# Optimization experiments

Hardware: AMD Instinct MI355X
Metric: run time of the kernel (lower is better)

The kernel has to match this reference:

```python
import jax, jax.numpy as jnp
import numpy as np

DIM = 1024
DEPTH = 2
HEADS = 16
MLP = 4096
HEAD_DIM = DIM // HEADS
EPS = 1e-5


def layernorm(x, w, b):
    mu = jnp.mean(x, axis=-1, keepdims=True)
    var = jnp.mean(jnp.square(x - mu), axis=-1, keepdims=True)
    return (x - mu) * jax.lax.rsqrt(var + EPS) * w + b


def setup_inputs() -> dict:
    key = jax.random.key(0)
    ks = jax.random.split(key, 16)
    s = 0.02
    x = jax.random.normal(ks[0], (2, 2048, DIM), dtype=jnp.float32)
    inp = {
        "x": x,
        "ln1_w": jnp.ones((DEPTH, DIM), jnp.float32),
        "ln1_b": jnp.zeros((DEPTH, DIM), jnp.float32),
        "qkv_w": jax.random.normal(ks[1], (DEPTH, DIM, 3 * DIM), jnp.float32) * s,
        "qkv_b": jnp.zeros((DEPTH, 3 * DIM), jnp.float32),
        "in_w": jax.random.normal(ks[2], (DEPTH, DIM, 3 * DIM), jnp.float32) * s,
        "in_b": jnp.zeros((DEPTH, 3 * DIM), jnp.float32),
        "out_w": jax.random.normal(ks[3], (DEPTH, DIM, DIM), jnp.float32) * s,
        "out_b": jnp.zeros((DEPTH, DIM), jnp.float32),
        "ln2_w": jnp.ones((DEPTH, DIM), jnp.float32),
        "ln2_b": jnp.zeros((DEPTH, DIM), jnp.float32),
        "w1": jax.random.normal(ks[4], (DEPTH, DIM, MLP), jnp.float32) * s,
        "b1": jnp.zeros((DEPTH, MLP), jnp.float32),
        "w2": jax.random.normal(ks[5], (DEPTH, MLP, DIM), jnp.float32) * s,
        "b2": jnp.zeros((DEPTH, DIM), jnp.float32),
    }
    return inp


def _forward(x, ln1_w, ln1_b, qkv_w, qkv_b, in_w, in_b, out_w, out_b,
             ln2_w, ln2_b, w1, b1, w2, b2):
    B, S, D = x.shape
    scale = 1.0 / jnp.sqrt(jnp.float32(HEAD_DIM))
    for i in range(DEPTH):
        # --- Attention block (pre-norm) ---
        h = layernorm(x, ln1_w[i], ln1_b[i])
        qkv = h @ qkv_w[i] + qkv_b[i]                      # [B,S,3D]
        q, k, v = jnp.split(qkv, 3, axis=-1)
        # nn.MultiheadAttention's own in_proj on top of to_qkv
        qp = q @ in_w[i][:, :D] + in_b[i][:D]
        kp = k @ in_w[i][:, D:2 * D] + in_b[i][D:2 * D]
        vp = v @ in_w[i][:, 2 * D:] + in_b[i][2 * D:]
        qp = qp.reshape(B, S, HEADS, HEAD_DIM)
        kp = kp.reshape(B, S, HEADS, HEAD_DIM)
        vp = vp.reshape(B, S, HEADS, HEAD_DIM)
        scores = jnp.einsum("bqhd,bkhd->bhqk", qp, kp) * scale
        attn = jax.nn.softmax(scores, axis=-1)
        o = jnp.einsum("bhqk,bkhd->bqhd", attn, vp).reshape(B, S, D)
        o = o @ out_w[i] + out_b[i]
        x = o + x
        # --- FFN block (pre-norm) ---
        h = layernorm(x, ln2_w[i], ln2_b[i])
        h = jax.nn.gelu(h @ w1[i] + b1[i], approximate=False)
        h = h @ w2[i] + b2[i]
        x = h + x
    return x


def reference(x, ln1_w, ln1_b, qkv_w, qkv_b, in_w, in_b, out_w, out_b,
              ln2_w, ln2_b, w1, b1, w2, b2):
    return _forward(x, ln1_w, ln1_b, qkv_w, qkv_b, in_w, in_b, out_w, out_b,
                    ln2_w, ln2_b, w1, b1, w2, b2)
```

## Files before the change

kernel.cpp:

```cpp
#include <hip/hip_runtime.h>
#include <math.h>

#define D_MODEL 1024
#define NHEADS 16
#define HEAD_DIM 64
#define SEQ 2048
#define BATCH 2
#define TOK (BATCH*SEQ)
#define MLP_DIM 4096

#define F_BIAS  1
#define F_GELU  2
#define QSCALE 0.18033688011112042f

typedef __attribute__((ext_vector_type(8))) __bf16 bf16x8;
typedef __attribute__((ext_vector_type(16))) __bf16 bf16x16;
typedef __attribute__((ext_vector_type(4))) __bf16 bf16x4;
typedef __attribute__((ext_vector_type(4))) float f32x4;

__device__ __forceinline__ void gload16(const void* g, void* l) {
    __builtin_amdgcn_global_load_lds(
        (const __attribute__((address_space(1))) void*)g,
        (__attribute__((address_space(3))) void*)l, 16, 0, 0);
}

__global__ __launch_bounds__(256)
void conv_kernel(const float* __restrict__ in, __bf16* __restrict__ out, int n8)
{
    const int idx = blockIdx.x * 256 + threadIdx.x;
    if (idx >= n8) return;
    const float4 a = *(const float4*)(in + idx * 8);
    const float4 b = *(const float4*)(in + idx * 8 + 4);
    bf16x8 o;
    o[0] = (__bf16)a.x; o[1] = (__bf16)a.y; o[2] = (__bf16)a.z; o[3] = (__bf16)a.w;
    o[4] = (__bf16)b.x; o[5] = (__bf16)b.y; o[6] = (__bf16)b.z; o[7] = (__bf16)b.w;
    *(bf16x8*)(out + idx * 8) = o;
}

__global__ __launch_bounds__(256)
void tconv64_kernel(const float* __restrict__ in, __bf16* __restrict__ out, int R, int C)
{
    __shared__ __bf16 tile[64][72];
    const int bx = blockIdx.x;
    const int by = blockIdx.y;
    const int t = threadIdx.x;
    const int rl = t >> 4, cl = (t & 15) * 4;
    #pragma unroll
    for (int rr = 0; rr < 4; ++rr) {
        const float4 v = *(const float4*)&in[(size_t)(by * 64 + rr * 16 + rl) * C + bx * 64 + cl];
        tile[rr * 16 + rl][cl + 0] = (__bf16)v.x;
        tile[rr * 16 + rl][cl + 1] = (__bf16)v.y;
        tile[rr * 16 + rl][cl + 2] = (__bf16)v.z;
        tile[rr * 16 + rl][cl + 3] = (__bf16)v.w;
    }
    __syncthreads();
    const int oc = t >> 2, rs = (t & 3) * 16;
    bf16x16 y;
    #pragma unroll
    for (int k = 0; k < 16; ++k) y[k] = tile[rs + k][oc];
    *(bf16x16*)&out[(size_t)(bx * 64 + oc) * R + by * 64 + rs] = y;
}

__global__ __launch_bounds__(256)
void bcomb_kernel(const float* __restrict__ qkv_b, const float* __restrict__ in_w,
                  const float* __restrict__ in_b, float* __restrict__ bc)
{
    const int t = blockIdx.x * 256 + threadIdx.x;
    const int p = t >> 10, n = t & 1023;
    float s = in_b[t];
    #pragma unroll 16
    for (int k = 0; k < D_MODEL; ++k)
        s = fmaf(qkv_b[p * D_MODEL + k], in_w[(size_t)k * 3 * D_MODEL + p * D_MODEL + n], s);
    bc[t] = s;
}

__global__ __launch_bounds__(256)
void tv_kernel(const __bf16* __restrict__ v, __bf16* __restrict__ vt)
{
    __shared__ __bf16 t[64][72];
    const int bh = blockIdx.y, b = bh >> 4, h = bh & 15;
    const int s0 = blockIdx.x * 64;
    const int r = threadIdx.x >> 3;
    const int c = (threadIdx.x & 7) * 8;
    #pragma unroll
    for (int rr = 0; rr < 64; rr += 32) {
        bf16x8 x = *(const bf16x8*)&v[(size_t)(b * SEQ + s0 + r + rr) * D_MODEL + h * 64 + c];
        #pragma unroll
        for (int k = 0; k < 8; ++k) t[r + rr][c + k] = x[k];
    }
    __syncthreads();
    #pragma unroll
    for (int rr = 0; rr < 64; rr += 32) {
        bf16x8 y;
        #pragma unroll
        for (int k = 0; k < 8; ++k) y[k] = t[c + k][r + rr];
        *(bf16x8*)&vt[((size_t)bh * 64 + r + rr) * SEQ + s0 + c] = y;
    }
}

__device__ __forceinline__ void ln_body(float4 v, const float* w, const float* b,
                                        __bf16* out, int row, int t)
{
    float s  = v.x + v.y + v.z + v.w;
    float ss = v.x*v.x + v.y*v.y + v.z*v.z + v.w*v.w;
    #pragma unroll
    for (int off = 32; off > 0; off >>= 1) {
        s  += __shfl_down(s, off);
        ss += __shfl_down(ss, off);
    }
    __shared__ float red[8];
    const int wid = t >> 6, lane = t & 63;
    if (lane == 0) { red[wid] = s; red[4 + wid] = ss; }
    __syncthreads();
    const float st  = red[0] + red[1] + red[2] + red[3];
    const float sst = red[4] + red[5] + red[6] + red[7];
    const float mu  = st * (1.0f / D_MODEL);
    const float var = sst * (1.0f / D_MODEL) - mu * mu;
    const float rs  = rsqrtf(var + 1e-5f);
    const float4 wv = *(const float4*)(w + t * 4);
    const float4 bv = *(const float4*)(b + t * 4);
    bf16x4 o;
    o[0] = (__bf16)((v.x - mu) * rs * wv.x + bv.x);
    o[1] = (__bf16)((v.y - mu) * rs * wv.y + bv.y);
    o[2] = (__bf16)((v.z - mu) * rs * wv.z + bv.z);
    o[3] = (__bf16)((v.w - mu) * rs * wv.w + bv.w);
    *(bf16x4*)(out + (size_t)row * D_MODEL + t * 4) = o;
}

__global__ __launch_bounds__(256)
void ln_kernel(const float* __restrict__ x, const float* __restrict__ w,
               const float* __restrict__ b, __bf16* __restrict__ out)
{
    const int row = blockIdx.x, t = threadIdx.x;
    float4 v = *(const float4*)(x + (size_t)row * D_MODEL + t * 4);
    ln_body(v, w, b, out, row, t);
}

__global__ __launch_bounds__(256)
void ln_add_kernel(float* __restrict__ x, const float* __restrict__ p0,
                   const float* __restrict__ p1, const float* __restrict__ w,
                   const float* __restrict__ b, __bf16* __restrict__ out)
{
    const int row = blockIdx.x, t = threadIdx.x;
    const size_t idx = (size_t)row * D_MODEL + t * 4;
    float4 v  = *(const float4*)(x + idx);
    float4 a0 = *(const float4*)(p0 + idx);
    float4 a1 = *(const float4*)(p1 + idx);
    v.x += a0.x + a1.x; v.y += a0.y + a1.y;
    v.z += a0.z + a1.z; v.w += a0.w + a1.w;
    *(float4*)(x + idx) = v;
    ln_body(v, w, b, out, row, t);
}

__global__ __launch_bounds__(256)
void add2_kernel(float* __restrict__ x, const float* __restrict__ p0,
                 const float* __restrict__ p1)
{
    const size_t idx = ((size_t)blockIdx.x * 256 + threadIdx.x) * 4;
    float4 v  = *(const float4*)(x + idx);
    float4 a0 = *(const float4*)(p0 + idx);
    float4 a1 = *(const float4*)(p1 + idx);
    v.x += a0.x + a1.x; v.y += a0.y + a1.y;
    v.z += a0.z + a1.z; v.w += a0.w + a1.w;
    *(float4*)(x + idx) = v;
}

template<int BN, int WM, int FLAGS, bool PROJ3, bool SPLITK, bool ZB>
__global__ __launch_bounds__(512)
void gs_kernel(const __bf16* __restrict__ A, int lda, long long sAz,
               const __bf16* __restrict__ Bt, int ldb, long long sBz,
               const float* __restrict__ bias,
               void* __restrict__ Cv, int ldc, int K, long long sCz)
{
    constexpr int WN = 8 / WM, RW = 256 / WM, CW = BN / WN;
    constexpr int MI = RW / 16, NJ = CW / 16;
    constexpr int LA = 4, LB = BN / 64;
    __shared__ __align__(16) __bf16 As[2][256 * 64];
    __shared__ __align__(16) __bf16 Bs[2][BN * 64];

    const int gx = gridDim.x;
    const int nwg = gx * gridDim.y;
    int lin = blockIdx.y * gx + blockIdx.x;
    lin = (lin & 7) * (nwg >> 3) + (lin >> 3);
    const int bm = lin / gx, bn = lin % gx;

    const int z = (SPLITK || ZB) ? blockIdx.z : 0;
    const __bf16* Ab = A  + (size_t)bm * 256 * lda
                          + (SPLITK ? (size_t)z * K : 0) + (ZB ? (size_t)z * sAz : 0);
    const __bf16* Bb = Bt + (size_t)bn * BN * ldb
                          + (SPLITK ? (size_t)z * K : 0) + (ZB ? (size_t)z * sBz : 0);

    const int tid = threadIdx.x, lane = tid & 63, w = tid >> 6;
    const int wm = w / WN, wn = w % WN;
    const int kq = lane >> 4, fr = lane & 15;
    const int l8 = lane >> 3;
    const int swz = (lane & 7) ^ l8;

    const __bf16* aPtr[LA]; int aLds[LA];
    #pragma unroll
    for (int c = 0; c < LA; ++c) {
        aPtr[c] = Ab + (size_t)(c * 64 + w * 8 + l8) * lda + swz * 8;
        aLds[c] = (c * 512 + w * 64) * 8;
    }
    const __bf16* bPtr[LB]; int bLds[LB];
    #pragma unroll
    for (int c = 0; c < LB; ++c) {
        bPtr[c] = Bb + (size_t)(c * 64 + w * 8 + l8) * ldb + swz * 8;
        bLds[c] = (c * 512 + w * 64) * 8;
    }

    f32x4 acc[MI][NJ];
    #pragma unroll
    for (int i = 0; i < MI; ++i)
        #pragma unroll
        for (int j = 0; j < NJ; ++j)
            acc[i][j] = (f32x4){0.f, 0.f, 0.f, 0.f};

    auto STG = [&](int buf, int k0) {
        #pragma unroll
        for (int c = 0; c < LA; ++c)
            gload16(aPtr[c] + k0, &As[buf][aLds[c]]);
        #pragma unroll
        for (int c = 0; c < LB; ++c)
            gload16(bPtr[c] + k0, &Bs[buf][bLds[c]]);
    };

    const int fsw = fr & 7;
    auto COMPUTE = [&](int buf) {
        #pragma unroll
        for (int kk = 0; kk < 2; ++kk) {
            const int kc = (kk * 4 + kq) ^ fsw;
            bf16x8 af[MI], bfr[NJ];
            #pragma unroll
            for (int i = 0; i < MI; ++i)
                af[i] = *(const bf16x8*)&As[buf][(wm * RW + i * 16 + fr) * 64 + kc * 8];
            #pragma unroll
            for (int j = 0; j < NJ; ++j)
                bfr[j] = *(const bf16x8*)&Bs[buf][(wn * CW + j * 16 + fr) * 64 + kc * 8];
            #pragma unroll
            for (int i = 0; i < MI; ++i)
                #pragma unroll
                for (int j = 0; j < NJ; ++j)
                    acc[i][j] = __builtin_amdgcn_mfma_f32_16x16x32_bf16(
                        af[i], bfr[j], acc[i][j], 0, 0, 0);
        }
    };

    const int T = K >> 6;
    STG(0, 0);
    __syncthreads();
    int cur = 0;
    for (int t = 0; t < T; ++t) {
        if (t + 1 < T) STG(cur ^ 1, (t + 1) * 64);
        COMPUTE(cur);
        __syncthreads();
        cur ^= 1;
    }

    const int row0 = bm * 256 + wm * RW + kq * 4;
    const int col0 = bn * BN + wn * CW + fr;
    if (SPLITK) {
        float* P = (float*)Cv + (size_t)z * sCz;
        #pragma unroll
        for (int i = 0; i < MI; ++i) {
            #pragma unroll
            for (int j = 0; j < NJ; ++j) {
                const int col = col0 + j * 16;
                const float bb = (z == 0) ? bias[col] : 0.0f;
                #pragma unroll
                for (int e = 0; e < 4; ++e)
                    P[(size_t)(row0 + i * 16 + e) * ldc + col] = acc[i][j][e] + bb;
            }
        }
    } else {
        __bf16* C = (__bf16*)Cv + (ZB ? (size_t)z * sCz : 0);
        #pragma unroll
        for (int i = 0; i < MI; ++i) {
            #pragma unroll
            for (int j = 0; j < NJ; ++j) {
                const int col = col0 + j * 16;
                const float bb = (FLAGS & F_BIAS) ? bias[col] : 0.0f;
                #pragma unroll
                for (int e = 0; e < 4; ++e) {
                    const int row = row0 + i * 16 + e;
                    float val = acc[i][j][e] + bb;
                    if (FLAGS & F_GELU)
                        val = 0.5f * val * (1.0f + erff(val * 0.70710678118654752f));
                    if (PROJ3) {
                        if ((col >> 10) == 0) val *= QSCALE;
                        C[(size_t)(col >> 10) * TOK * D_MODEL +
                          (size_t)row * D_MODEL + (col & 1023)] = (__bf16)val;
                    } else {
                        C[(size_t)row * ldc + col] = (__bf16)val;
                    }
                }
            }
        }
    }
}

__global__ __launch_bounds__(256)
void attn7_kernel(const __bf16* __restrict__ qp, const __bf16* __restrict__ kp,
                  const __bf16* __restrict__ vt, __bf16* __restrict__ o)
{
    const int bh = blockIdx.y;
    const int b = bh >> 4, h = bh & 15;
    const int tid = threadIdx.x;
    const int lane = tid & 63;
    const int w = tid >> 6;
    const int g = lane >> 4;
    const int fr = lane & 15;
    const int q0 = blockIdx.x * 64 + w * 16;
    const int l8 = lane >> 3, swz = (lane & 7) ^ l8, fsw = fr & 7;

    __shared__ __align__(16) __bf16 Ks[2][64 * 64];
    __shared__ __align__(16) __bf16 Vs[2][64 * 64];
    __shared__ __align__(16) __bf16 Ps[4][16 * 72];

    const __bf16* qb = qp + (size_t)(b * SEQ + q0 + fr) * D_MODEL + h * HEAD_DIM;
    const bf16x8 qf0 = *(const bf16x8*)(qb + g * 8);
    const bf16x8 qf1 = *(const bf16x8*)(qb + 32 + g * 8);

    const __bf16* kb = kp + (size_t)(b * SEQ) * D_MODEL + h * HEAD_DIM;
    const __bf16* vb = vt + (size_t)bh * HEAD_DIM * SEQ;

    const __bf16* kPtr[2]; const __bf16* vPtr[2]; int sLds[2];
    #pragma unroll
    for (int c = 0; c < 2; ++c) {
        const int row = c * 32 + w * 8 + l8;
        kPtr[c] = kb + (size_t)row * D_MODEL + swz * 8;
        vPtr[c] = vb + (size_t)row * SEQ + swz * 8;
        sLds[c] = (c * 256 + w * 64) * 8;
    }

    auto STG = [&](int buf, int kv0) {
        #pragma unroll
        for (int c = 0; c < 2; ++c)
            gload16(kPtr[c] + (size_t)kv0 * D_MODEL, &Ks[buf][sLds[c]]);
        #pragma unroll
        for (int c = 0; c < 2; ++c)
            gload16(vPtr[c] + kv0, &Vs[buf][sLds[c]]);
    };

    f32x4 acc_o[4];
    #pragma unroll
    for (int dj = 0; dj < 4; ++dj) acc_o[dj] = (f32x4){0.f, 0.f, 0.f, 0.f};
    float l_lane = 0.0f;

    STG(0, 0);
    __syncthreads();
    int tb = 0;
    for (int kv0 = 0; kv0 < SEQ; kv0 += 64) {
        if (kv0 + 64 < SEQ) STG(tb ^ 1, kv0 + 64);

        f32x4 sacc[4];
        __builtin_amdgcn_s_setprio(1);
        #pragma unroll
        for (int t = 0; t < 4; ++t) {
            const bf16x8 kf0 = *(const bf16x8*)&Ks[tb][(t * 16 + fr) * 64 + ((g    ) ^ fsw) * 8];
            const bf16x8 kf1 = *(const bf16x8*)&Ks[tb][(t * 16 + fr) * 64 + ((4 + g) ^ fsw) * 8];
            sacc[t] = __builtin_amdgcn_mfma_f32_16x16x32_bf16(
                kf0, qf0, (f32x4){0.f, 0.f, 0.f, 0.f}, 0, 0, 0);
            sacc[t] = __builtin_amdgcn_mfma_f32_16x16x32_bf16(kf1, qf1, sacc[t], 0, 0, 0);
        }
        __builtin_amdgcn_s_setprio(0);

        #pragma unroll
        for (int t = 0; t < 4; ++t) {
            bf16x4 pv;
            #pragma unroll
            for (int e = 0; e < 4; ++e) {
                const float p = __builtin_amdgcn_exp2f(sacc[t][e]);
                l_lane += p;
                pv[e] = (__bf16)p;
            }
            *(bf16x4*)&Ps[w][fr * 72 + t * 16 + g * 4] = pv;
        }

        __builtin_amdgcn_s_setprio(1);
        #pragma unroll
        for (int c = 0; c < 2; ++c) {
            const bf16x8 pf = *(const bf16x8*)&Ps[w][fr * 72 + c * 32 + g * 8];
            #pragma unroll
            for (int dj = 0; dj < 4; ++dj) {
                const bf16x8 vf = *(const bf16x8*)&Vs[tb][(dj * 16 + fr) * 64 +
                                                         ((c * 4 + g) ^ fsw) * 8];
                acc_o[dj] = __builtin_amdgcn_mfma_f32_16x16x32_bf16(vf, pf, acc_o[dj], 0, 0, 0);
            }
        }
        __builtin_amdgcn_s_setprio(0);
        __syncthreads();
        tb ^= 1;
    }

    l_lane += __shfl_xor(l_lane, 16);
    l_lane += __shfl_xor(l_lane, 32);
    const float inv = 1.0f / l_lane;
    __bf16* orow = o + (size_t)(b * SEQ + q0 + fr) * D_MODEL + h * HEAD_DIM;
    #pragma unroll
    for (int dj = 0; dj < 4; ++dj) {
        bf16x4 t;
        #pragma unroll
        for (int e = 0; e < 4; ++e) t[e] = (__bf16)(acc_o[dj][e] * inv);
        *(bf16x4*)&orow[dj * 16 + g * 4] = t;
    }
}

extern "C" void kernel_launch(void* const* d_in, const int* in_sizes, int n_in,
                              void* d_out, int out_size, void* d_ws, size_t ws_size,
                              hipStream_t stream)
{
    const float* x    = (const float*)d_in[0];
    const float* ln1w = (const float*)d_in[1];
    const float* ln1b = (const float*)d_in[2];
    const float* qkvw = (const float*)d_in[3];
    const float* qkvb = (const float*)d_in[4];
    const float* inw  = (const float*)d_in[5];
    const float* inb  = (const float*)d_in[6];
    const float* outw = (const float*)d_in[7];
    const float* outb = (const float*)d_in[8];
    const float* ln2w = (const float*)d_in[9];
    const float* ln2b = (const float*)d_in[10];
    const float* w1   = (const float*)d_in[11];
    const float* b1   = (const float*)d_in[12];
    const float* w2   = (const float*)d_in[13];
    const float* b2   = (const float*)d_in[14];
    float* xo = (float*)d_out;

    const size_t OFF_WCT = 0;
    const size_t OFF_OUT = 3145728;
    const size_t OFF_W1  = 4194304;
    const size_t OFF_W2  = 8388608;
    const size_t L_WT    = 12582912;

    __bf16* WT   = (__bf16*)d_ws;
    __bf16* QKVb = WT + 2 * L_WT;
    __bf16* INt  = QKVb + 3145728;
    __bf16* X8   = INt + 3145728;
    __bf16* U_   = X8 + 4194304;
    __bf16* QKV3 = U_ + 16777216;
    __bf16* VT   = QKV3 + 12582912;
    float*  BC   = (float*)(VT + 4194304);
    float*  P_   = (float*)QKV3;

    hipMemcpyAsync(xo, x, (size_t)TOK * D_MODEL * sizeof(float),
                   hipMemcpyDeviceToDevice, stream);

    const dim3 blk(256);
    for (int i = 0; i < 2; ++i) {
        __bf16* wl = WT + i * L_WT;
        const float* l_qkvw = qkvw + (size_t)i * D_MODEL * 3 * D_MODEL;
        const float* l_inw  = inw  + (size_t)i * D_MODEL * 3 * D_MODEL;
        conv_kernel<<<1536, blk, 0, stream>>>(l_qkvw, QKVb, 393216);
        tconv64_kernel<<<dim3(48, 16), blk, 0, stream>>>(l_inw, INt, D_MODEL, 3 * D_MODEL);
        gs_kernel<256, 2, 0, false, false, true><<<dim3(4, 4, 3), 512, 0, stream>>>(
            INt, D_MODEL, 1048576LL, QKVb, 3 * D_MODEL, (long long)D_MODEL,
            nullptr, wl + OFF_WCT, D_MODEL, D_MODEL, 1048576LL);
        bcomb_kernel<<<12, blk, 0, stream>>>(
            qkvb + (size_t)i * 3 * D_MODEL, l_inw, inb + (size_t)i * 3 * D_MODEL,
            BC + (size_t)i * 3 * D_MODEL);
        tconv64_kernel<<<dim3(16, 16), blk, 0, stream>>>(
            outw + (size_t)i * D_MODEL * D_MODEL, wl + OFF_OUT, D_MODEL, D_MODEL);
        tconv64_kernel<<<dim3(64, 16), blk, 0, stream>>>(
            w1 + (size_t)i * D_MODEL * MLP_DIM, wl + OFF_W1, D_MODEL, MLP_DIM);
        tconv64_kernel<<<dim3(16, 64), blk, 0, stream>>>(
            w2 + (size_t)i * MLP_DIM * D_MODEL, wl + OFF_W2, MLP_DIM, D_MODEL);
    }

    for (int i = 0; i < 2; ++i) {
        __bf16* wl = WT + i * L_WT;
        const float* l_outb = outb + (size_t)i * D_MODEL;
        const float* l_b1   = b1   + (size_t)i * MLP_DIM;
        const float* l_b2   = b2   + (size_t)i * D_MODEL;

        if (i == 0)
            ln_kernel<<<TOK, blk, 0, stream>>>(xo, ln1w, ln1b, X8);
        gs_kernel<256, 2, F_BIAS, true, false, false><<<dim3(12, 16), 512, 0, stream>>>(
            X8, D_MODEL, 0, wl + OFF_WCT, D_MODEL, 0,
            BC + (size_t)i * 3 * D_MODEL, QKV3, D_MODEL, D_MODEL, 0);
        tv_kernel<<<dim3(SEQ / 64, BATCH * NHEADS), blk, 0, stream>>>(
            QKV3 + (size_t)2 * TOK * D_MODEL, VT);
        attn7_kernel<<<dim3(SEQ / 64, BATCH * NHEADS), blk, 0, stream>>>(
            QKV3, QKV3 + (size_t)TOK * D_MODEL, VT, X8);
        gs_kernel<128, 4, F_BIAS, false, true, false><<<dim3(8, 16, 2), 512, 0, stream>>>(
            X8, D_MODEL, 0, wl + OFF_OUT, D_MODEL, 0, l_outb, P_, D_MODEL, 512,
            (long long)TOK * D_MODEL);
        ln_add_kernel<<<TOK, blk, 0, stream>>>(
            xo, P_, P_ + (size_t)TOK * D_MODEL,
            ln2w + (size_t)i * D_MODEL, ln2b + (size_t)i * D_MODEL, X8);
        gs_kernel<256, 2, F_BIAS | F_GELU, false, false, false><<<dim3(16, 16), 512, 0, stream>>>(
            X8, D_MODEL, 0, wl + OFF_W1, D_MODEL, 0, l_b1, U_, MLP_DIM, D_MODEL, 0);
        gs_kernel<128, 4, F_BIAS, false, true, false><<<dim3(8, 16, 2), 512, 0, stream>>>(
            U_, MLP_DIM, 0, wl + OFF_W2, MLP_DIM, 0, l_b2, P_, D_MODEL, 2048,
            (long long)TOK * D_MODEL);
        if (i == 0) {
            ln_add_kernel<<<TOK, blk, 0, stream>>>(
                xo, P_, P_ + (size_t)TOK * D_MODEL,
                ln1w + D_MODEL, ln1b + D_MODEL, X8);
        } else {
            add2_kernel<<<TOK * D_MODEL / 1024, blk, 0, stream>>>(
                xo, P_, P_ + (size_t)TOK * D_MODEL);
        }
    }
}
```

Baseline: 737.4 us.

## Halve GEMM K-tile to 32 and process two query tiles per attention block

The GEMM kernel's K-step drops from 64 to 32. This halves shared-memory use per buffer and changes the LDS XOR swizzle to match the narrower rows, which may allow more resident workgroups but doubles the loop iterations and barriers. The attention kernel now handles 128 queries per block as two 64-query halves that share each staged K/V tile. This halves K/V global and LDS traffic per query and gives the matrix units more independent work, at the cost of more registers and half as many blocks in the grid.

```diff
diff --git a/kernel.cpp b/kernel.cpp
--- a/kernel.cpp
+++ b/kernel.cpp
@@ -174,9 +174,9 @@
 {
     constexpr int WN = 8 / WM, RW = 256 / WM, CW = BN / WN;
     constexpr int MI = RW / 16, NJ = CW / 16;
-    constexpr int LA = 4, LB = BN / 64;
-    __shared__ __align__(16) __bf16 As[2][256 * 64];
-    __shared__ __align__(16) __bf16 Bs[2][BN * 64];
+    constexpr int LA = 2, LB = BN / 128;
+    __shared__ __align__(16) __bf16 As[2][256 * 32];
+    __shared__ __align__(16) __bf16 Bs[2][BN * 32];
 
     const int gx = gridDim.x;
     const int nwg = gx * gridDim.y;
@@ -193,20 +193,20 @@
     const int tid = threadIdx.x, lane = tid & 63, w = tid >> 6;
     const int wm = w / WN, wn = w % WN;
     const int kq = lane >> 4, fr = lane & 15;
-    const int l8 = lane >> 3;
-    const int swz = (lane & 7) ^ l8;
 
     const __bf16* aPtr[LA]; int aLds[LA];
     #pragma unroll
     for (int c = 0; c < LA; ++c) {
-        aPtr[c] = Ab + (size_t)(c * 64 + w * 8 + l8) * lda + swz * 8;
-        aLds[c] = (c * 512 + w * 64) * 8;
+        const int s = c * 512 + tid;
+        aPtr[c] = Ab + (size_t)(s >> 2) * lda + (((s & 3) ^ ((s >> 2) & 3)) * 8);
+        aLds[c] = s * 8;
     }
     const __bf16* bPtr[LB]; int bLds[LB];
     #pragma unroll
     for (int c = 0; c < LB; ++c) {
-        bPtr[c] = Bb + (size_t)(c * 64 + w * 8 + l8) * ldb + swz * 8;
-        bLds[c] = (c * 512 + w * 64) * 8;
+        const int s = c * 512 + tid;
+        bPtr[c] = Bb + (size_t)(s >> 2) * ldb + (((s & 3) ^ ((s >> 2) & 3)) * 8);
+        bLds[c] = s * 8;
     }
 
     f32x4 acc[MI][NJ];
@@ -225,33 +225,29 @@
             gload16(bPtr[c] + k0, &Bs[buf][bLds[c]]);
     };
 
-    const int fsw = fr & 7;
+    const int kc = kq ^ (fr & 3);
     auto COMPUTE = [&](int buf) {
-        #pragma unroll
-        for (int kk = 0; kk < 2; ++kk) {
-            const int kc = (kk * 4 + kq) ^ fsw;
-            bf16x8 af[MI], bfr[NJ];
-            #pragma unroll
-            for (int i = 0; i < MI; ++i)
-                af[i] = *(const bf16x8*)&As[buf][(wm * RW + i * 16 + fr) * 64 + kc * 8];
+        bf16x8 af[MI], bfr[NJ];
+        #pragma unroll
+        for (int i = 0; i < MI; ++i)
+            af[i] = *(const bf16x8*)&As[buf][(wm * RW + i * 16 + fr) * 32 + kc * 8];
+        #pragma unroll
+        for (int j = 0; j < NJ; ++j)
+            bfr[j] = *(const bf16x8*)&Bs[buf][(wn * CW + j * 16 + fr) * 32 + kc * 8];
+        #pragma unroll
+        for (int i = 0; i < MI; ++i)
             #pragma unroll
             for (int j = 0; j < NJ; ++j)
-                bfr[j] = *(const bf16x8*)&Bs[buf][(wn * CW + j * 16 + fr) * 64 + kc * 8];
-            #pragma unroll
-            for (int i = 0; i < MI; ++i)
-                #pragma unroll
-                for (int j = 0; j < NJ; ++j)
-                    acc[i][j] = __builtin_amdgcn_mfma_f32_16x16x32_bf16(
-                        af[i], bfr[j], acc[i][j], 0, 0, 0);
-        }
+                acc[i][j] = __builtin_amdgcn_mfma_f32_16x16x32_bf16(
+                    af[i], bfr[j], acc[i][j], 0, 0, 0);
     };
 
-    const int T = K >> 6;
+    const int T = K >> 5;
     STG(0, 0);
     __syncthreads();
     int cur = 0;
     for (int t = 0; t < T; ++t) {
-        if (t + 1 < T) STG(cur ^ 1, (t + 1) * 64);
+        if (t + 1 < T) STG(cur ^ 1, (t + 1) * 32);
         COMPUTE(cur);
         __syncthreads();
         cur ^= 1;
@@ -300,7 +296,7 @@
 }
 
 __global__ __launch_bounds__(256)
-void attn7_kernel(const __bf16* __restrict__ qp, const __bf16* __restrict__ kp,
+void attn8_kernel(const __bf16* __restrict__ qp, const __bf16* __restrict__ kp,
                   const __bf16* __restrict__ vt, __bf16* __restrict__ o)
 {
     const int bh = blockIdx.y;
@@ -310,16 +306,20 @@
     const int w = tid >> 6;
     const int g = lane >> 4;
     const int fr = lane & 15;
-    const int q0 = blockIdx.x * 64 + w * 16;
+    const int q0 = blockIdx.x * 128 + w * 16;
     const int l8 = lane >> 3, swz = (lane & 7) ^ l8, fsw = fr & 7;
 
     __shared__ __align__(16) __bf16 Ks[2][64 * 64];
     __shared__ __align__(16) __bf16 Vs[2][64 * 64];
-    __shared__ __align__(16) __bf16 Ps[4][16 * 72];
-
-    const __bf16* qb = qp + (size_t)(b * SEQ + q0 + fr) * D_MODEL + h * HEAD_DIM;
-    const bf16x8 qf0 = *(const bf16x8*)(qb + g * 8);
-    const bf16x8 qf1 = *(const bf16x8*)(qb + 32 + g * 8);
+    __shared__ __align__(16) __bf16 PsA[4][16 * 72];
+    __shared__ __align__(16) __bf16 PsB[4][16 * 72];
+
+    const __bf16* qbA = qp + (size_t)(b * SEQ + q0 + fr) * D_MODEL + h * HEAD_DIM;
+    const __bf16* qbB = qbA + (size_t)64 * D_MODEL;
+    const bf16x8 qfA0 = *(const bf16x8*)(qbA + g * 8);
+    const bf16x8 qfA1 = *(const bf16x8*)(qbA + 32 + g * 8);
+    const bf16x8 qfB0 = *(const bf16x8*)(qbB + g * 8);
+    const bf16x8 qfB1 = *(const bf16x8*)(qbB + 32 + g * 8);
 
     const __bf16* kb = kp + (size_t)(b * SEQ) * D_MODEL + h * HEAD_DIM;
     const __bf16* vb = vt + (size_t)bh * HEAD_DIM * SEQ;
@@ -342,10 +342,13 @@
             gload16(vPtr[c] + kv0, &Vs[buf][sLds[c]]);
     };
 
-    f32x4 acc_o[4];
-    #pragma unroll
-    for (int dj = 0; dj < 4; ++dj) acc_o[dj] = (f32x4){0.f, 0.f, 0.f, 0.f};
-    float l_lane = 0.0f;
+    f32x4 acc_oA[4], acc_oB[4];
+    #pragma unroll
+    for (int dj = 0; dj < 4; ++dj) {
+        acc_oA[dj] = (f32x4){0.f, 0.f, 0.f, 0.f};
+        acc_oB[dj] = (f32x4){0.f, 0.f, 0.f, 0.f};
+    }
+    float l_A = 0.0f, l_B = 0.0f;
 
     STG(0, 0);
     __syncthreads();
@@ -353,39 +356,46 @@
     for (int kv0 = 0; kv0 < SEQ; kv0 += 64) {
         if (kv0 + 64 < SEQ) STG(tb ^ 1, kv0 + 64);
 
-        f32x4 sacc[4];
+        f32x4 sA[4], sB[4];
         __builtin_amdgcn_s_setprio(1);
         #pragma unroll
         for (int t = 0; t < 4; ++t) {
             const bf16x8 kf0 = *(const bf16x8*)&Ks[tb][(t * 16 + fr) * 64 + ((g    ) ^ fsw) * 8];
             const bf16x8 kf1 = *(const bf16x8*)&Ks[tb][(t * 16 + fr) * 64 + ((4 + g) ^ fsw) * 8];
-            sacc[t] = __builtin_amdgcn_mfma_f32_16x16x32_bf16(
-                kf0, qf0, (f32x4){0.f, 0.f, 0.f, 0.f}, 0, 0, 0);
-            sacc[t] = __builtin_amdgcn_mfma_f32_16x16x32_bf16(kf1, qf1, sacc[t], 0, 0, 0);
+            sA[t] = __builtin_amdgcn_mfma_f32_16x16x32_bf16(
+                kf0, qfA0, (f32x4){0.f, 0.f, 0.f, 0.f}, 0, 0, 0);
+            sA[t] = __builtin_amdgcn_mfma_f32_16x16x32_bf16(kf1, qfA1, sA[t], 0, 0, 0);
+            sB[t] = __builtin_amdgcn_mfma_f32_16x16x32_bf16(
+                kf0, qfB0, (f32x4){0.f, 0.f, 0.f, 0.f}, 0, 0, 0);
+            sB[t] = __builtin_amdgcn_mfma_f32_16x16x32_bf16(kf1, qfB1, sB[t], 0, 0, 0);
         }
         __builtin_amdgcn_s_setprio(0);
 
         #pragma unroll
         for (int t = 0; t < 4; ++t) {
-            bf16x4 pv;
+            bf16x4 pvA, pvB;
             #pragma unroll
             for (int e = 0; e < 4; ++e) {
-                const float p = __builtin_amdgcn_exp2f(sacc[t][e]);
-                l_lane += p;
-                pv[e] = (__bf16)p;
+                const float pA = __builtin_amdgcn_exp2f(sA[t][e]);
+                const float pB = __builtin_amdgcn_exp2f(sB[t][e]);
+                l_A += pA; l_B += pB;
+                pvA[e] = (__bf16)pA; pvB[e] = (__bf16)pB;
             }
-            *(bf16x4*)&Ps[w][fr * 72 + t * 16 + g * 4] = pv;
+            *(bf16x4*)&PsA[w][fr * 72 + t * 16 + g * 4] = pvA;
+            *(bf16x4*)&PsB[w][fr * 72 + t * 16 + g * 4] = pvB;
         }
 
         __builtin_amdgcn_s_setprio(1);
         #pragma unroll
         for (int c = 0; c < 2; ++c) {
-            const bf16x8 pf = *(const bf16x8*)&Ps[w][fr * 72 + c * 32 + g * 8];
+            const bf16x8 pfA = *(const bf16x8*)&PsA[w][fr * 72 + c * 32 + g * 8];
+            const bf16x8 pfB = *(const bf16x8*)&PsB[w][fr * 72 + c * 32 + g * 8];
             #pragma unroll
             for (int dj = 0; dj < 4; ++dj) {
                 const bf16x8 vf = *(const bf16x8*)&Vs[tb][(dj * 16 + fr) * 64 +
                                                          ((c * 4 + g) ^ fsw) * 8];
-                acc_o[dj] = __builtin_amdgcn_mfma_f32_16x16x32_bf16(vf, pf, acc_o[dj], 0, 0, 0);
+                acc_oA[dj] = __builtin_amdgcn_mfma_f32_16x16x32_bf16(vf, pfA, acc_oA[dj], 0, 0, 0);
+                acc_oB[dj] = __builtin_amdgcn_mfma_f32_16x16x32_bf16(vf, pfB, acc_oB[dj], 0, 0, 0);
             }
         }
         __builtin_amdgcn_s_setprio(0);
@@ -393,16 +403,21 @@
         tb ^= 1;
     }
 
-    l_lane += __shfl_xor(l_lane, 16);
-    l_lane += __shfl_xor(l_lane, 32);
-    const float inv = 1.0f / l_lane;
-    __bf16* orow = o + (size_t)(b * SEQ + q0 + fr) * D_MODEL + h * HEAD_DIM;
+    l_A += __shfl_xor(l_A, 16); l_A += __shfl_xor(l_A, 32);
+    l_B += __shfl_xor(l_B, 16); l_B += __shfl_xor(l_B, 32);
+    const float invA = 1.0f / l_A, invB = 1.0f / l_B;
+    __bf16* orowA = o + (size_t)(b * SEQ + q0 + fr) * D_MODEL + h * HEAD_DIM;
+    __bf16* orowB = orowA + (size_t)64 * D_MODEL;
     #pragma unroll
     for (int dj = 0; dj < 4; ++dj) {
-        bf16x4 t;
-        #pragma unroll
-        for (int e = 0; e < 4; ++e) t[e] = (__bf16)(acc_o[dj][e] * inv);
-        *(bf16x4*)&orow[dj * 16 + g * 4] = t;
+        bf16x4 tA, tB;
+        #pragma unroll
+        for (int e = 0; e < 4; ++e) {
+            tA[e] = (__bf16)(acc_oA[dj][e] * invA);
+            tB[e] = (__bf16)(acc_oB[dj][e] * invB);
+        }
+        *(bf16x4*)&orowA[dj * 16 + g * 4] = tA;
+        *(bf16x4*)&orowB[dj * 16 + g * 4] = tB;
     }
 }
 
@@ -480,7 +495,7 @@
             BC + (size_t)i * 3 * D_MODEL, QKV3, D_MODEL, D_MODEL, 0);
         tv_kernel<<<dim3(SEQ / 64, BATCH * NHEADS), blk, 0, stream>>>(
             QKV3 + (size_t)2 * TOK * D_MODEL, VT);
-        attn7_kernel<<<dim3(SEQ / 64, BATCH * NHEADS), blk, 0, stream>>>(
+        attn8_kernel<<<dim3(SEQ / 128, BATCH * NHEADS), blk, 0, stream>>>(
             QKV3, QKV3 + (size_t)TOK * D_MODEL, VT, X8);
         gs_kernel<128, 4, F_BIAS, false, true, false><<<dim3(8, 16, 2), 512, 0, stream>>>(
             X8, D_MODEL, 0, wl + OFF_OUT, D_MODEL, 0, l_outb, P_, D_MODEL, 512,
```

After: 764.1 us. 1.04x slower.
